# Kernel tuning notes

Measured on AMD Instinct MI355X. Metric: run time of the kernel, lower is better.

Reference implementation:

```python
import jax, jax.numpy as jnp
import numpy as np

N_NODES = 100000
IN_DIM = 128
N_HEADS = 4
D_HEAD = 32
N_EDGES = 800000
LN_EPS = 1e-5
NEG_SLOPE = 0.2


def setup_inputs() -> dict:
    key = jax.random.key(0)
    k = jax.random.split(key, 7)
    x = jax.random.normal(k[0], (N_NODES, IN_DIM), dtype=jnp.float32)
    edge_index = jax.random.randint(k[1], (2, N_EDGES), 0, N_NODES, dtype=jnp.int32)
    # W: Linear(in_dim, H*D, bias=False) -> store as [in_dim, H*D] for x @ W
    W = jax.random.normal(k[2], (IN_DIM, N_HEADS * D_HEAD), dtype=jnp.float32) * (1.0 / np.sqrt(IN_DIM))
    # attn_mlp: Linear(2*D, 1, bias=False), shared across heads; split into src/dst halves
    a_src = jax.random.normal(k[3], (D_HEAD,), dtype=jnp.float32) * 0.1
    a_dst = jax.random.normal(k[4], (D_HEAD,), dtype=jnp.float32) * 0.1
    ln_gamma = jnp.ones((N_HEADS * D_HEAD,), dtype=jnp.float32)
    ln_beta = jnp.zeros((N_HEADS * D_HEAD,), dtype=jnp.float32)
    return {"x": x, "edge_index": edge_index, "W": W, "a_src": a_src,
            "a_dst": a_dst, "ln_gamma": ln_gamma, "ln_beta": ln_beta}


def reference(x, edge_index, W, a_src, a_dst, ln_gamma, ln_beta):
    N = x.shape[0]
    # dense projection: [N, H*D] -> [N, H, D]
    h = (x @ W).reshape(N, N_HEADS, D_HEAD)
    src, dst = edge_index[0], edge_index[1]
    h_src = h[src]          # [E, H, D] gather
    h_dst = h[dst]          # [E, H, D] gather
    # attn_mlp(cat([h_src, h_dst])) == h_src @ a[:D] + h_dst @ a[D:]
    s = jnp.einsum('ehd,d->eh', h_src, a_src) + jnp.einsum('ehd,d->eh', h_dst, a_dst)
    s = jnp.where(s > 0, s, NEG_SLOPE * s)  # LeakyReLU(0.2)
    # segment softmax over destination node groups (per head)
    smax = jax.ops.segment_max(s, dst, num_segments=N)          # [N, H]
    e = jnp.exp(s - smax[dst])                                   # [E, H]
    denom = jax.ops.segment_sum(e, dst, num_segments=N)          # [N, H]
    alpha = e / denom[dst]                                       # [E, H]
    # weighted scatter-add aggregation
    msg = h_src * alpha[..., None]                               # [E, H, D]
    out = jax.ops.segment_sum(msg, dst, num_segments=N)          # [N, H, D]
    out = out.reshape(N, N_HEADS * D_HEAD)
    # residual: in_dim == H*D -> Identity
    out = out + x
    # LayerNorm
    mu = out.mean(-1, keepdims=True)
    var = ((out - mu) ** 2).mean(-1, keepdims=True)
    out = (out - mu) / jnp.sqrt(var + LN_EPS) * ln_gamma + ln_beta
    # ELU
    return jnp.where(out > 0, out, jnp.expm1(out))
```

## Files before the change

kernel.cpp:

```cpp
#include <hip/hip_runtime.h>
#include <math.h>

#define NEG_SLOPE 0.2f
#define LN_EPS 1e-5f

#define NB 196
#define EPB 2048

typedef __attribute__((ext_vector_type(8))) short bf16x8;
typedef __attribute__((ext_vector_type(4))) float f32x4;

static __device__ __forceinline__ unsigned short f2bf(float f) {
  unsigned u = __float_as_uint(f);
  u += 0x7fffu + ((u >> 16) & 1u);
  return (unsigned short)(u >> 16);
}
static __device__ __forceinline__ unsigned pack_bf16(float a, float b) {
  unsigned ua = __float_as_uint(a);
  unsigned ub = __float_as_uint(b);
  ua += 0x7fffu + ((ua >> 16) & 1u);
  ub += 0x7fffu + ((ub >> 16) & 1u);
  return (ua >> 16) | (ub & 0xffff0000u);
}
static __device__ __forceinline__ float bf_lo(unsigned u) { return __uint_as_float(u << 16); }
static __device__ __forceinline__ float bf_hi(unsigned u) { return __uint_as_float(u & 0xffff0000u); }

__global__ __launch_bounds__(256) void k_prep(
    const float* __restrict__ W, const float* __restrict__ a_src,
    const float* __restrict__ a_dst, short* __restrict__ wfrag,
    short* __restrict__ wafrag)
{
  const int t = threadIdx.x;
  if (blockIdx.x < 8) {
    const int idx  = blockIdx.x * 256 + t;
    const int tile = idx >> 6;
    const int l2   = idx & 63;
    const int c    = tile >> 2;
    const int kk   = tile & 3;
    const int q2   = l2 >> 4;
    const int i2   = l2 & 15;
    const float* wp = W + (size_t)(kk * 32 + q2 * 8) * 128 + c * 16 + i2;
    bf16x8 wv;
    #pragma unroll
    for (int j = 0; j < 8; ++j) wv[j] = (short)f2bf(wp[(size_t)j * 128]);
    *(bf16x8*)(wfrag + (size_t)idx * 8) = wv;
  } else {
    const int kk = t >> 6;
    const int l2 = t & 63;
    const int q2 = l2 >> 4;
    const int i2 = l2 & 15;
    bf16x8 wv = {0, 0, 0, 0, 0, 0, 0, 0};
    if (i2 < 8) {
      const int head = i2 >> 1;
      const float* ap = (i2 & 1) ? a_dst : a_src;
      #pragma unroll
      for (int j = 0; j < 8; ++j) {
        const int k = kk * 32 + q2 * 8 + j;
        const float* wr = W + (size_t)k * 128 + head * 32;
        float sum = 0.f;
        for (int d = 0; d < 32; d += 4) {
          const float4 wq = *(const float4*)(wr + d);
          const float4 aq = *(const float4*)(ap + d);
          sum += wq.x * aq.x + wq.y * aq.y + wq.z * aq.z + wq.w * aq.w;
        }
        wv[j] = (short)f2bf(sum);
      }
    }
    *(bf16x8*)(wafrag + (size_t)t * 8) = wv;
  }
}

__global__ __launch_bounds__(256) void k_bhist(
    const int* __restrict__ e_dst, int* __restrict__ H, int n_edges, int nblk)
{
  __shared__ int hist[NB];
  const int t = threadIdx.x;
  if (t < NB) hist[t] = 0;
  __syncthreads();
  int e = blockIdx.x * EPB + t * 8;
  if (e + 8 <= n_edges) {
    const int4 d0 = *(const int4*)(e_dst + e);
    const int4 d1 = *(const int4*)(e_dst + e + 4);
    atomicAdd(&hist[d0.x >> 9], 1); atomicAdd(&hist[d0.y >> 9], 1);
    atomicAdd(&hist[d0.z >> 9], 1); atomicAdd(&hist[d0.w >> 9], 1);
    atomicAdd(&hist[d1.x >> 9], 1); atomicAdd(&hist[d1.y >> 9], 1);
    atomicAdd(&hist[d1.z >> 9], 1); atomicAdd(&hist[d1.w >> 9], 1);
  } else {
    const int eend = (e + 8 < n_edges) ? (e + 8) : n_edges;
    for (; e < eend; ++e) atomicAdd(&hist[e_dst[e] >> 9], 1);
  }
  __syncthreads();
  if (t < NB) H[t * nblk + blockIdx.x] = hist[t];
}

__global__ __launch_bounds__(256) void k_cscan(
    int* __restrict__ H, int* __restrict__ totals, int nblk)
{
  __shared__ int sdata[256];
  const int b = blockIdx.x, t = threadIdx.x;
  int* col = H + (size_t)b * nblk;
  const int i0 = 2 * t, i1 = 2 * t + 1;
  const int v0 = (i0 < nblk) ? col[i0] : 0;
  const int v1 = (i1 < nblk) ? col[i1] : 0;
  const int tsum = v0 + v1;
  sdata[t] = tsum;
  __syncthreads();
  for (int off = 1; off < 256; off <<= 1) {
    const int addv = (t >= off) ? sdata[t - off] : 0;
    __syncthreads();
    sdata[t] += addv;
    __syncthreads();
  }
  const int excl = sdata[t] - tsum;
  if (i0 < nblk) col[i0] = excl;
  if (i1 < nblk) col[i1] = excl + v0;
  if (t == 255) totals[b] = sdata[255];
}

__global__ __launch_bounds__(256) void k_scatter(
    const int* __restrict__ e_src, const int* __restrict__ e_dst,
    const int* __restrict__ H, const int* __restrict__ totals,
    int2* __restrict__ ebuf, int n_edges, int nblk)
{
  __shared__ int sdata[256];
  __shared__ int cur[NB];
  const int t = threadIdx.x;
  const int tv = (t < NB) ? totals[t] : 0;
  sdata[t] = tv;
  __syncthreads();
  for (int off = 1; off < 256; off <<= 1) {
    const int addv = (t >= off) ? sdata[t - off] : 0;
    __syncthreads();
    sdata[t] += addv;
    __syncthreads();
  }
  if (t < NB) cur[t] = (sdata[t] - tv) + H[t * nblk + blockIdx.x];
  __syncthreads();
  int e = blockIdx.x * EPB + t * 8;
  if (e + 8 <= n_edges) {
    const int4 d0 = *(const int4*)(e_dst + e);
    const int4 d1 = *(const int4*)(e_dst + e + 4);
    const int4 s0 = *(const int4*)(e_src + e);
    const int4 s1 = *(const int4*)(e_src + e + 4);
    int p;
    p = atomicAdd(&cur[d0.x >> 9], 1); ebuf[p] = make_int2(d0.x, s0.x);
    p = atomicAdd(&cur[d0.y >> 9], 1); ebuf[p] = make_int2(d0.y, s0.y);
    p = atomicAdd(&cur[d0.z >> 9], 1); ebuf[p] = make_int2(d0.z, s0.z);
    p = atomicAdd(&cur[d0.w >> 9], 1); ebuf[p] = make_int2(d0.w, s0.w);
    p = atomicAdd(&cur[d1.x >> 9], 1); ebuf[p] = make_int2(d1.x, s1.x);
    p = atomicAdd(&cur[d1.y >> 9], 1); ebuf[p] = make_int2(d1.y, s1.y);
    p = atomicAdd(&cur[d1.z >> 9], 1); ebuf[p] = make_int2(d1.z, s1.z);
    p = atomicAdd(&cur[d1.w >> 9], 1); ebuf[p] = make_int2(d1.w, s1.w);
  } else {
    const int eend = (e + 8 < n_edges) ? (e + 8) : n_edges;
    for (; e < eend; ++e) {
      const int d = e_dst[e];
      const int p = atomicAdd(&cur[d >> 9], 1);
      ebuf[p] = make_int2(d, e_src[e]);
    }
  }
}

__global__ __launch_bounds__(256) void k_bcsr(
    const int2* __restrict__ ebuf, const int* __restrict__ totals,
    int* __restrict__ row_start, int* __restrict__ csr_src, int n_nodes)
{
  __shared__ int sdata[256];
  __shared__ int hist[512];
  __shared__ int cur[512];
  const int b = blockIdx.x, t = threadIdx.x;
  const int n0 = b << 9;

  const int tv = (t < NB) ? totals[t] : 0;
  sdata[t] = tv;
  __syncthreads();
  for (int off = 1; off < 256; off <<= 1) {
    const int addv = (t >= off) ? sdata[t - off] : 0;
    __syncthreads();
    sdata[t] += addv;
    __syncthreads();
  }
  const int base = (b == 0) ? 0 : sdata[b - 1];
  const int nE   = sdata[b] - base;

  hist[t] = 0; hist[t + 256] = 0;
  __syncthreads();
  for (int e = t; e < nE; e += 256)
    atomicAdd(&hist[ebuf[base + e].x - n0], 1);
  __syncthreads();

  const int h0 = hist[2 * t], h1 = hist[2 * t + 1];
  const int tsum = h0 + h1;
  sdata[t] = tsum;
  __syncthreads();
  for (int off = 1; off < 256; off <<= 1) {
    const int addv = (t >= off) ? sdata[t - off] : 0;
    __syncthreads();
    sdata[t] += addv;
    __syncthreads();
  }
  const int excl = sdata[t] - tsum;
  cur[2 * t]     = excl;
  cur[2 * t + 1] = excl + h0;
  if (n0 + 2 * t     <= n_nodes) row_start[n0 + 2 * t]     = base + excl;
  if (n0 + 2 * t + 1 <= n_nodes) row_start[n0 + 2 * t + 1] = base + excl + h0;
  __syncthreads();

  for (int e = t; e < nE; e += 256) {
    const int2 ds = ebuf[base + e];
    const int r = atomicAdd(&cur[ds.x - n0], 1);
    csr_src[base + r] = ds.y;
  }
}

__global__ __launch_bounds__(256, 4) void k_proj(
    const float* __restrict__ x, const short* __restrict__ wfrag,
    const short* __restrict__ wafrag,
    unsigned* __restrict__ h, float* __restrict__ sc, int n_nodes)
{
  __shared__ __align__(16) short wlds[32 * 64 * 8];
  __shared__ __align__(16) short walds[4 * 64 * 8];

  const int t    = threadIdx.x;
  const int l    = t & 63;
  const int il   = l & 15;
  const int quad = l >> 4;
  const int wbase = blockIdx.x * 128 + (t >> 6) * 32;

  {
    const uint4* wf4 = (const uint4*)wfrag;
    uint4* wl4 = (uint4*)wlds;
    #pragma unroll
    for (int i = 0; i < 8; ++i) wl4[t + i * 256] = wf4[t + i * 256];
    ((uint4*)walds)[t] = ((const uint4*)wafrag)[t];
  }
  __syncthreads();

  f32x4 acc[2][8] = {};
  f32x4 acc2[2] = {};
  #pragma unroll
  for (int kk = 0; kk < 4; ++kk) {
    bf16x8 ahi[2], alo[2];
    #pragma unroll
    for (int rt = 0; rt < 2; ++rt) {
      int row = wbase + rt * 16 + il;
      if (row > n_nodes - 1) row = n_nodes - 1;
      const float* p = x + (size_t)row * 128 + kk * 32 + quad * 8;
      const float4 u0 = *(const float4*)(p);
      const float4 u1 = *(const float4*)(p + 4);
      const float f[8] = {u0.x, u0.y, u0.z, u0.w, u1.x, u1.y, u1.z, u1.w};
      #pragma unroll
      for (int j = 0; j < 8; ++j) {
        const unsigned u = __float_as_uint(f[j]);
        ahi[rt][j] = (short)(u >> 16);
        const float lof = f[j] - __uint_as_float(u & 0xffff0000u);
        alo[rt][j] = (short)f2bf(lof);
      }
    }
    #pragma unroll
    for (int c = 0; c < 8; ++c) {
      const bf16x8 bv = *(const bf16x8*)(wlds + ((c * 4 + kk) * 64 + l) * 8);
      acc[0][c] = __builtin_amdgcn_mfma_f32_16x16x32_bf16(ahi[0], bv, acc[0][c], 0, 0, 0);
      acc[0][c] = __builtin_amdgcn_mfma_f32_16x16x32_bf16(alo[0], bv, acc[0][c], 0, 0, 0);
      acc[1][c] = __builtin_amdgcn_mfma_f32_16x16x32_bf16(ahi[1], bv, acc[1][c], 0, 0, 0);
      acc[1][c] = __builtin_amdgcn_mfma_f32_16x16x32_bf16(alo[1], bv, acc[1][c], 0, 0, 0);
    }
    const bf16x8 bv = *(const bf16x8*)(walds + (kk * 64 + l) * 8);
    acc2[0] = __builtin_amdgcn_mfma_f32_16x16x32_bf16(ahi[0], bv, acc2[0], 0, 0, 0);
    acc2[0] = __builtin_amdgcn_mfma_f32_16x16x32_bf16(alo[0], bv, acc2[0], 0, 0, 0);
    acc2[1] = __builtin_amdgcn_mfma_f32_16x16x32_bf16(ahi[1], bv, acc2[1], 0, 0, 0);
    acc2[1] = __builtin_amdgcn_mfma_f32_16x16x32_bf16(alo[1], bv, acc2[1], 0, 0, 0);
  }

  #pragma unroll
  for (int rt = 0; rt < 2; ++rt) {
    #pragma unroll
    for (int reg = 0; reg < 4; ++reg) {
      const int r = wbase + rt * 16 + quad * 4 + reg;
      const bool inb = (r < n_nodes);
      const bool wr = inb && ((il & 3) == 0);
      #pragma unroll
      for (int c = 0; c < 8; ++c) {
        const float v  = acc[rt][c][reg];
        const float vn = __shfl_xor(v, 1);
        const float plo = (il & 1) ? vn : v;
        const float phi = (il & 1) ? v : vn;
        const unsigned px = pack_bf16(plo, phi);
        const unsigned py = __shfl_xor(px, 2);
        if (wr) {
          uint2 u; u.x = px; u.y = py;
          *(uint2*)(h + (size_t)r * 64 + c * 8 + (il >> 1)) = u;
        }
      }
      if (inb && il < 8) sc[(size_t)r * 8 + il] = acc2[rt][reg];
    }
  }
}

#define ACC_EDGE(al, hv)                              \
  acc[0] = fmaf(al, bf_lo(hv.x), acc[0]);             \
  acc[1] = fmaf(al, bf_hi(hv.x), acc[1]);             \
  acc[2] = fmaf(al, bf_lo(hv.y), acc[2]);             \
  acc[3] = fmaf(al, bf_hi(hv.y), acc[3]);             \
  acc[4] = fmaf(al, bf_lo(hv.z), acc[4]);             \
  acc[5] = fmaf(al, bf_hi(hv.z), acc[5]);             \
  acc[6] = fmaf(al, bf_lo(hv.w), acc[6]);             \
  acc[7] = fmaf(al, bf_hi(hv.w), acc[7]);

__global__ __launch_bounds__(256) void k_agg(
    const unsigned* __restrict__ h, const float* __restrict__ sc,
    const int* __restrict__ row_start, const int* __restrict__ csr_src,
    const float* __restrict__ x, const float* __restrict__ gamma,
    const float* __restrict__ beta, float* __restrict__ out, int n_nodes)
{
  const int t    = threadIdx.x;
  const int lane = t & 63;
  const int g    = lane & 15;
  const int node = blockIdx.x * 16 + (t >> 6) * 4 + (lane >> 4);
  if (node >= n_nodes) return;
  const int head = g >> 2;
  const int sub  = g & 3;
  const int hh   = head * 2;
  const int beg  = row_start[node];
  const int deg  = row_start[node + 1] - beg;
  const float sdv = sc[node * 8 + hh + 1];

  float m = -INFINITY, l = 0.f;
  float t0 = 0.f, t1 = 0.f, t2 = 0.f, t3 = 0.f;
  int   c0 = 0,   c1 = 0,   c2 = 0,   c3 = 0;
  if (sub < deg) {
    c0 = csr_src[beg + sub];
    float s = sc[c0 * 8 + hh] + sdv;  s = s > 0.f ? s : NEG_SLOPE * s;
    t0 = s; m = s; l = 1.f;
  }
  if (sub + 4 < deg) {
    c1 = csr_src[beg + sub + 4];
    float s = sc[c1 * 8 + hh] + sdv;  s = s > 0.f ? s : NEG_SLOPE * s;
    t1 = s;
    const float mn = fmaxf(m, s);
    l = l * __expf(m - mn) + __expf(s - mn);  m = mn;
  }
  if (sub + 8 < deg) {
    c2 = csr_src[beg + sub + 8];
    float s = sc[c2 * 8 + hh] + sdv;  s = s > 0.f ? s : NEG_SLOPE * s;
    t2 = s;
    const float mn = fmaxf(m, s);
    l = l * __expf(m - mn) + __expf(s - mn);  m = mn;
  }
  if (sub + 12 < deg) {
    c3 = csr_src[beg + sub + 12];
    float s = sc[c3 * 8 + hh] + sdv;  s = s > 0.f ? s : NEG_SLOPE * s;
    t3 = s;
    const float mn = fmaxf(m, s);
    l = l * __expf(m - mn) + __expf(s - mn);  m = mn;
  }
  for (int i = sub + 16; i < deg; i += 4) {
    const int cs = csr_src[beg + i];
    float s = sc[cs * 8 + hh] + sdv;  s = s > 0.f ? s : NEG_SLOPE * s;
    const float mn = fmaxf(m, s);
    l = l * __expf(m - mn) + __expf(s - mn);  m = mn;
  }
  #pragma unroll
  for (int off = 1; off < 4; off <<= 1) {
    const float m2 = __shfl_xor(m, off);
    const float l2 = __shfl_xor(l, off);
    const float mn = fmaxf(m, m2);
    if (mn == -INFINITY) { m = -INFINITY; l = 0.f; }
    else {
      l = l * __expf(m - mn) + l2 * __expf(m2 - mn);
      m = mn;
    }
  }
  const float inv_l = (deg > 0) ? 1.f / l : 0.f;
  const float a0 = __expf(t0 - m) * inv_l;
  const float a1 = __expf(t1 - m) * inv_l;
  const float a2 = __expf(t2 - m) * inv_l;
  const float a3 = __expf(t3 - m) * inv_l;

  const int base3 = lane & 60;

  float acc[8] = {0.f, 0.f, 0.f, 0.f, 0.f, 0.f, 0.f, 0.f};
  const int deg16 = deg < 16 ? deg : 16;
  #pragma unroll
  for (int r = 0; r < 4; ++r) {
    const int i0 = r * 4;
    if (i0 >= deg16) break;
    const float ar = r == 0 ? a0 : r == 1 ? a1 : r == 2 ? a2 : a3;
    const int   cr = r == 0 ? c0 : r == 1 ? c1 : r == 2 ? c2 : c3;
    const int   n  = deg16 - i0;
    {
      const float al = __shfl(ar, base3 | 0);
      const int   sr = __shfl(cr, base3 | 0);
      const uint4 hv = *(const uint4*)(h + (size_t)sr * 64 + g * 4);
      ACC_EDGE(al, hv)
    }
    if (n > 1) {
      const float al = __shfl(ar, base3 | 1);
      const int   sr = __shfl(cr, base3 | 1);
      const uint4 hv = *(const uint4*)(h + (size_t)sr * 64 + g * 4);
      ACC_EDGE(al, hv)
    }
    if (n > 2) {
      const float al = __shfl(ar, base3 | 2);
      const int   sr = __shfl(cr, base3 | 2);
      const uint4 hv = *(const uint4*)(h + (size_t)sr * 64 + g * 4);
      ACC_EDGE(al, hv)
    }
    if (n > 3) {
      const float al = __shfl(ar, base3 | 3);
      const int   sr = __shfl(cr, base3 | 3);
      const uint4 hv = *(const uint4*)(h + (size_t)sr * 64 + g * 4);
      ACC_EDGE(al, hv)
    }
  }
  for (int i = 16; i < deg; ++i) {
    const int sr = csr_src[beg + i];
    float s = sc[sr * 8 + hh] + sdv;  s = s > 0.f ? s : NEG_SLOPE * s;
    const float al = __expf(s - m) * inv_l;
    const uint4 hv = *(const uint4*)(h + (size_t)sr * 64 + g * 4);
    ACC_EDGE(al, hv)
  }

  const float4 xa = *(const float4*)(x + (size_t)node * 128 + g * 8);
  const float4 xb = *(const float4*)(x + (size_t)node * 128 + g * 8 + 4);
  float rr[8];
  rr[0] = acc[0] + xa.x;  rr[1] = acc[1] + xa.y;
  rr[2] = acc[2] + xa.z;  rr[3] = acc[3] + xa.w;
  rr[4] = acc[4] + xb.x;  rr[5] = acc[5] + xb.y;
  rr[6] = acc[6] + xb.z;  rr[7] = acc[7] + xb.w;
  float s1 = 0.f, s2 = 0.f;
  #pragma unroll
  for (int j = 0; j < 8; ++j) { s1 += rr[j]; s2 += rr[j] * rr[j]; }
  #pragma unroll
  for (int off = 1; off < 16; off <<= 1) {
    s1 += __shfl_xor(s1, off);
    s2 += __shfl_xor(s2, off);
  }
  const float mu   = s1 * (1.f / 128.f);
  const float var  = s2 * (1.f / 128.f) - mu * mu;
  const float rstd = rsqrtf(var + LN_EPS);
  const float4 ga = *(const float4*)(gamma + g * 8);
  const float4 gb = *(const float4*)(gamma + g * 8 + 4);
  const float4 ba = *(const float4*)(beta  + g * 8);
  const float4 bb = *(const float4*)(beta  + g * 8 + 4);
  float4 o0, o1;
  o0.x = (rr[0] - mu) * rstd * ga.x + ba.x;
  o0.y = (rr[1] - mu) * rstd * ga.y + ba.y;
  o0.z = (rr[2] - mu) * rstd * ga.z + ba.z;
  o0.w = (rr[3] - mu) * rstd * ga.w + ba.w;
  o1.x = (rr[4] - mu) * rstd * gb.x + bb.x;
  o1.y = (rr[5] - mu) * rstd * gb.y + bb.y;
  o1.z = (rr[6] - mu) * rstd * gb.z + bb.z;
  o1.w = (rr[7] - mu) * rstd * gb.w + bb.w;
  o0.x = o0.x > 0.f ? o0.x : expm1f(o0.x);
  o0.y = o0.y > 0.f ? o0.y : expm1f(o0.y);
  o0.z = o0.z > 0.f ? o0.z : expm1f(o0.z);
  o0.w = o0.w > 0.f ? o0.w : expm1f(o0.w);
  o1.x = o1.x > 0.f ? o1.x : expm1f(o1.x);
  o1.y = o1.y > 0.f ? o1.y : expm1f(o1.y);
  o1.z = o1.z > 0.f ? o1.z : expm1f(o1.z);
  o1.w = o1.w > 0.f ? o1.w : expm1f(o1.w);
  *(float4*)(out + (size_t)node * 128 + g * 8)     = o0;
  *(float4*)(out + (size_t)node * 128 + g * 8 + 4) = o1;
}

extern "C" void kernel_launch(void* const* d_in, const int* in_sizes, int n_in,
                              void* d_out, int out_size, void* d_ws, size_t ws_size,
                              hipStream_t stream)
{
  const float* x    = (const float*)d_in[0];
  const int*   ei   = (const int*)d_in[1];
  const float* W    = (const float*)d_in[2];
  const float* a_s  = (const float*)d_in[3];
  const float* a_d  = (const float*)d_in[4];
  const float* gam  = (const float*)d_in[5];
  const float* bet  = (const float*)d_in[6];
  float* out = (float*)d_out;

  const int n_nodes = in_sizes[0] / 128;
  const int n_edges = in_sizes[1] / 2;
  const int* e_src = ei;
  const int* e_dst = ei + n_edges;

  const int nblkE = (n_edges + EPB - 1) / EPB;

  char* p = (char*)d_ws;
  unsigned* h = (unsigned*)p; p += (size_t)n_nodes * 64 * sizeof(unsigned);
  float* sc   = (float*)p;  p += (size_t)n_nodes * 8 * sizeof(float);
  int* row_start = (int*)p; p += (size_t)(n_nodes + 4) * sizeof(int);
  int* csr_src   = (int*)p; p += (size_t)n_edges * sizeof(int);
  short* wfrag   = (short*)p; p += (size_t)2048 * 8 * sizeof(short);
  short* wafrag  = (short*)p; p += (size_t)256 * 8 * sizeof(short);
  int* H      = (int*)p; p += (size_t)NB * nblkE * sizeof(int);
  int* totals = (int*)p; p += (size_t)NB * sizeof(int);
  int2* ebuf  = (int2*)h;

  k_prep<<<9, 256, 0, stream>>>(W, a_s, a_d, wfrag, wafrag);
  k_bhist<<<nblkE, 256, 0, stream>>>(e_dst, H, n_edges, nblkE);
  k_cscan<<<NB, 256, 0, stream>>>(H, totals, nblkE);
  k_scatter<<<nblkE, 256, 0, stream>>>(e_src, e_dst, H, totals, ebuf, n_edges, nblkE);
  k_bcsr<<<NB, 256, 0, stream>>>(ebuf, totals, row_start, csr_src, n_nodes);
  const int nproj = (n_nodes + 127) / 128;
  k_proj<<<nproj, 256, 0, stream>>>(x, wfrag, wafrag, h, sc, n_nodes);
  k_agg<<<(n_nodes + 15) / 16, 256, 0, stream>>>(h, sc, row_start, csr_src, x, gam, bet, out, n_nodes);
}
```

Baseline: 207.5 us.

## Fuse CSR build and projection into one cooperative kernel; two-pass softmax

Merges the prep, histogram, scan, scatter, per-bucket CSR and projection kernels into a single cooperative persistent kernel that separates phases with grid-wide syncs and reuses one shared-memory buffer. The aim is to remove several kernel launch gaps and tail effects. The projection tiles now run in a grid-stride loop over a fixed grid, which may cause load imbalance. The aggregation kernel swaps its online softmax for a max pass then a sum pass, which trades the rescaling exps for a second gather of neighbour scores. It also uses nontemporal loads for x and nontemporal stores for the output.

Measured after the change: 476.3 us. +129.5%, slower.

```diff
diff --git a/kernel.cpp b/kernel.cpp
--- a/kernel.cpp
+++ b/kernel.cpp
@@ -1,4 +1,5 @@
 #include <hip/hip_runtime.h>
+#include <hip/hip_cooperative_groups.h>
 #include <math.h>
 
 #define NEG_SLOPE 0.2f
@@ -6,6 +7,9 @@
 
 #define NB 196
 #define EPB 2048
+#define SMEM_BYTES (36 * 1024)
+
+namespace cg = cooperative_groups;
 
 typedef __attribute__((ext_vector_type(8))) short bf16x8;
 typedef __attribute__((ext_vector_type(4))) float f32x4;
@@ -25,14 +29,15 @@
 static __device__ __forceinline__ float bf_lo(unsigned u) { return __uint_as_float(u << 16); }
 static __device__ __forceinline__ float bf_hi(unsigned u) { return __uint_as_float(u & 0xffff0000u); }
 
-__global__ __launch_bounds__(256) void k_prep(
+
+static __device__ __forceinline__ void prep_body(
     const float* __restrict__ W, const float* __restrict__ a_src,
     const float* __restrict__ a_dst, short* __restrict__ wfrag,
-    short* __restrict__ wafrag)
+    short* __restrict__ wafrag, int bid)
 {
   const int t = threadIdx.x;
-  if (blockIdx.x < 8) {
-    const int idx  = blockIdx.x * 256 + t;
+  if (bid < 8) {
+    const int idx  = bid * 256 + t;
     const int tile = idx >> 6;
     const int l2   = idx & 63;
     const int c    = tile >> 2;
@@ -70,14 +75,15 @@
   }
 }
 
-__global__ __launch_bounds__(256) void k_bhist(
-    const int* __restrict__ e_dst, int* __restrict__ H, int n_edges, int nblk)
-{
-  __shared__ int hist[NB];
+static __device__ __forceinline__ void bhist_body(
+    const int* __restrict__ e_dst, int* __restrict__ H, int n_edges, int nblk,
+    int b, char* smem)
+{
+  int* hist = (int*)smem;
   const int t = threadIdx.x;
   if (t < NB) hist[t] = 0;
   __syncthreads();
-  int e = blockIdx.x * EPB + t * 8;
+  int e = b * EPB + t * 8;
   if (e + 8 <= n_edges) {
     const int4 d0 = *(const int4*)(e_dst + e);
     const int4 d1 = *(const int4*)(e_dst + e + 4);
@@ -90,14 +96,14 @@
     for (; e < eend; ++e) atomicAdd(&hist[e_dst[e] >> 9], 1);
   }
   __syncthreads();
-  if (t < NB) H[t * nblk + blockIdx.x] = hist[t];
-}
-
-__global__ __launch_bounds__(256) void k_cscan(
-    int* __restrict__ H, int* __restrict__ totals, int nblk)
-{
-  __shared__ int sdata[256];
-  const int b = blockIdx.x, t = threadIdx.x;
+  if (t < NB) H[t * nblk + b] = hist[t];
+}
+
+static __device__ __forceinline__ void cscan_body(
+    int* __restrict__ H, int* __restrict__ totals, int nblk, int b, char* smem)
+{
+  int* sdata = (int*)smem;
+  const int t = threadIdx.x;
   int* col = H + (size_t)b * nblk;
   const int i0 = 2 * t, i1 = 2 * t + 1;
   const int v0 = (i0 < nblk) ? col[i0] : 0;
@@ -117,13 +123,13 @@
   if (t == 255) totals[b] = sdata[255];
 }
 
-__global__ __launch_bounds__(256) void k_scatter(
+static __device__ __forceinline__ void scatter_body(
     const int* __restrict__ e_src, const int* __restrict__ e_dst,
     const int* __restrict__ H, const int* __restrict__ totals,
-    int2* __restrict__ ebuf, int n_edges, int nblk)
-{
-  __shared__ int sdata[256];
-  __shared__ int cur[NB];
+    int2* __restrict__ ebuf, int n_edges, int nblk, int b, char* smem)
+{
+  int* sdata = (int*)smem;
+  int* cur   = (int*)(smem + 1024);
   const int t = threadIdx.x;
   const int tv = (t < NB) ? totals[t] : 0;
   sdata[t] = tv;
@@ -134,9 +140,9 @@
     sdata[t] += addv;
     __syncthreads();
   }
-  if (t < NB) cur[t] = (sdata[t] - tv) + H[t * nblk + blockIdx.x];
-  __syncthreads();
-  int e = blockIdx.x * EPB + t * 8;
+  if (t < NB) cur[t] = (sdata[t] - tv) + H[t * nblk + b];
+  __syncthreads();
+  int e = b * EPB + t * 8;
   if (e + 8 <= n_edges) {
     const int4 d0 = *(const int4*)(e_dst + e);
     const int4 d1 = *(const int4*)(e_dst + e + 4);
@@ -161,14 +167,15 @@
   }
 }
 
-__global__ __launch_bounds__(256) void k_bcsr(
+static __device__ __forceinline__ void bcsr_body(
     const int2* __restrict__ ebuf, const int* __restrict__ totals,
-    int* __restrict__ row_start, int* __restrict__ csr_src, int n_nodes)
-{
-  __shared__ int sdata[256];
-  __shared__ int hist[512];
-  __shared__ int cur[512];
-  const int b = blockIdx.x, t = threadIdx.x;
+    int* __restrict__ row_start, int* __restrict__ csr_src, int n_nodes,
+    int b, char* smem)
+{
+  int* sdata = (int*)smem;
+  int* hist  = (int*)(smem + 1024);
+  int* cur   = (int*)(smem + 1024 + 2048);
+  const int t = threadIdx.x;
   const int n0 = b << 9;
 
   const int tv = (t < NB) ? totals[t] : 0;
@@ -213,28 +220,32 @@
   }
 }
 
-__global__ __launch_bounds__(256, 4) void k_proj(
-    const float* __restrict__ x, const short* __restrict__ wfrag,
-    const short* __restrict__ wafrag,
-    unsigned* __restrict__ h, float* __restrict__ sc, int n_nodes)
-{
-  __shared__ __align__(16) short wlds[32 * 64 * 8];
-  __shared__ __align__(16) short walds[4 * 64 * 8];
+static __device__ __forceinline__ void proj_stage(
+    const short* __restrict__ wfrag, const short* __restrict__ wafrag,
+    char* smem)
+{
+  short* wlds  = (short*)smem;
+  short* walds = (short*)(smem + 32 * 1024);
+  const int t = threadIdx.x;
+  const uint4* wf4 = (const uint4*)wfrag;
+  uint4* wl4 = (uint4*)wlds;
+  #pragma unroll
+  for (int i = 0; i < 8; ++i) wl4[t + i * 256] = wf4[t + i * 256];
+  ((uint4*)walds)[t] = ((const uint4*)wafrag)[t];
+}
+
+static __device__ __forceinline__ void proj_compute(
+    const float* __restrict__ x, unsigned* __restrict__ h,
+    float* __restrict__ sc, int n_nodes, int pb, char* smem)
+{
+  short* wlds  = (short*)smem;
+  short* walds = (short*)(smem + 32 * 1024);
 
   const int t    = threadIdx.x;
   const int l    = t & 63;
   const int il   = l & 15;
   const int quad = l >> 4;
-  const int wbase = blockIdx.x * 128 + (t >> 6) * 32;
-
-  {
-    const uint4* wf4 = (const uint4*)wfrag;
-    uint4* wl4 = (uint4*)wlds;
-    #pragma unroll
-    for (int i = 0; i < 8; ++i) wl4[t + i * 256] = wf4[t + i * 256];
-    ((uint4*)walds)[t] = ((const uint4*)wafrag)[t];
-  }
-  __syncthreads();
+  const int wbase = pb * 128 + (t >> 6) * 32;
 
   f32x4 acc[2][8] = {};
   f32x4 acc2[2] = {};
@@ -297,6 +308,41 @@
   }
 }
 
+__global__ __launch_bounds__(256, 4) void k_csrproj(
+    const float* __restrict__ W, const float* __restrict__ a_src,
+    const float* __restrict__ a_dst, short* __restrict__ wfrag,
+    short* __restrict__ wafrag,
+    const int* __restrict__ e_src, const int* __restrict__ e_dst,
+    int* __restrict__ H, int* __restrict__ totals, int2* __restrict__ ebuf,
+    int* __restrict__ row_start, int* __restrict__ csr_src,
+    const float* __restrict__ x, unsigned* __restrict__ h,
+    float* __restrict__ sc, int n_nodes, int n_edges, int nblk, int nproj)
+{
+  __shared__ __align__(16) char smem[SMEM_BYTES];
+  cg::grid_group grid = cg::this_grid();
+
+  if ((int)blockIdx.x < 9) prep_body(W, a_src, a_dst, wfrag, wafrag, blockIdx.x);
+  else if ((int)blockIdx.x < 9 + nblk)
+    bhist_body(e_dst, H, n_edges, nblk, blockIdx.x - 9, smem);
+  grid.sync();
+
+  if ((int)blockIdx.x < NB) cscan_body(H, totals, nblk, blockIdx.x, smem);
+  grid.sync();
+
+  if ((int)blockIdx.x < nblk)
+    scatter_body(e_src, e_dst, H, totals, ebuf, n_edges, nblk, blockIdx.x, smem);
+  grid.sync();
+
+  if ((int)blockIdx.x < NB)
+    bcsr_body(ebuf, totals, row_start, csr_src, n_nodes, blockIdx.x, smem);
+  grid.sync();
+
+  proj_stage(wfrag, wafrag, smem);
+  __syncthreads();
+  for (int u = blockIdx.x; u < nproj; u += gridDim.x)
+    proj_compute(x, h, sc, n_nodes, u, smem);
+}
+
 #define ACC_EDGE(al, hv)                              \
   acc[0] = fmaf(al, bf_lo(hv.x), acc[0]);             \
   acc[1] = fmaf(al, bf_hi(hv.x), acc[1]);             \
@@ -325,57 +371,48 @@
   const int deg  = row_start[node + 1] - beg;
   const float sdv = sc[node * 8 + hh + 1];
 
-  float m = -INFINITY, l = 0.f;
-  float t0 = 0.f, t1 = 0.f, t2 = 0.f, t3 = 0.f;
-  int   c0 = 0,   c1 = 0,   c2 = 0,   c3 = 0;
+  float t0 = -INFINITY, t1 = -INFINITY, t2 = -INFINITY, t3 = -INFINITY;
+  int   c0 = 0,          c1 = 0,          c2 = 0,          c3 = 0;
   if (sub < deg) {
     c0 = csr_src[beg + sub];
-    float s = sc[c0 * 8 + hh] + sdv;  s = s > 0.f ? s : NEG_SLOPE * s;
-    t0 = s; m = s; l = 1.f;
+    float s = sc[c0 * 8 + hh] + sdv;  t0 = s > 0.f ? s : NEG_SLOPE * s;
   }
   if (sub + 4 < deg) {
     c1 = csr_src[beg + sub + 4];
-    float s = sc[c1 * 8 + hh] + sdv;  s = s > 0.f ? s : NEG_SLOPE * s;
-    t1 = s;
-    const float mn = fmaxf(m, s);
-    l = l * __expf(m - mn) + __expf(s - mn);  m = mn;
+    float s = sc[c1 * 8 + hh] + sdv;  t1 = s > 0.f ? s : NEG_SLOPE * s;
   }
   if (sub + 8 < deg) {
     c2 = csr_src[beg + sub + 8];
-    float s = sc[c2 * 8 + hh] + sdv;  s = s > 0.f ? s : NEG_SLOPE * s;
-    t2 = s;
-    const float mn = fmaxf(m, s);
-    l = l * __expf(m - mn) + __expf(s - mn);  m = mn;
+    float s = sc[c2 * 8 + hh] + sdv;  t2 = s > 0.f ? s : NEG_SLOPE * s;
   }
   if (sub + 12 < deg) {
     c3 = csr_src[beg + sub + 12];
-    float s = sc[c3 * 8 + hh] + sdv;  s = s > 0.f ? s : NEG_SLOPE * s;
-    t3 = s;
-    const float mn = fmaxf(m, s);
-    l = l * __expf(m - mn) + __expf(s - mn);  m = mn;
-  }
+    float s = sc[c3 * 8 + hh] + sdv;  t3 = s > 0.f ? s : NEG_SLOPE * s;
+  }
+  float m = fmaxf(fmaxf(t0, t1), fmaxf(t2, t3));
   for (int i = sub + 16; i < deg; i += 4) {
     const int cs = csr_src[beg + i];
     float s = sc[cs * 8 + hh] + sdv;  s = s > 0.f ? s : NEG_SLOPE * s;
-    const float mn = fmaxf(m, s);
-    l = l * __expf(m - mn) + __expf(s - mn);  m = mn;
-  }
-  #pragma unroll
-  for (int off = 1; off < 4; off <<= 1) {
-    const float m2 = __shfl_xor(m, off);
-    const float l2 = __shfl_xor(l, off);
-    const float mn = fmaxf(m, m2);
-    if (mn == -INFINITY) { m = -INFINITY; l = 0.f; }
-    else {
-      l = l * __expf(m - mn) + l2 * __expf(m2 - mn);
-      m = mn;
-    }
-  }
+    m = fmaxf(m, s);
+  }
+  m = fmaxf(m, __shfl_xor(m, 1));
+  m = fmaxf(m, __shfl_xor(m, 2));
+
+  const float e0 = __expf(t0 - m), e1 = __expf(t1 - m);
+  const float e2 = __expf(t2 - m), e3 = __expf(t3 - m);
+  float l = e0 + e1 + e2 + e3;
+  for (int i = sub + 16; i < deg; i += 4) {
+    const int cs = csr_src[beg + i];
+    float s = sc[cs * 8 + hh] + sdv;  s = s > 0.f ? s : NEG_SLOPE * s;
+    l += __expf(s - m);
+  }
+  l += __shfl_xor(l, 1);
+  l += __shfl_xor(l, 2);
   const float inv_l = (deg > 0) ? 1.f / l : 0.f;
-  const float a0 = __expf(t0 - m) * inv_l;
-  const float a1 = __expf(t1 - m) * inv_l;
-  const float a2 = __expf(t2 - m) * inv_l;
-  const float a3 = __expf(t3 - m) * inv_l;
+  const float a0 = e0 * inv_l;
+  const float a1 = e1 * inv_l;
+  const float a2 = e2 * inv_l;
+  const float a3 = e3 * inv_l;
 
   const int base3 = lane & 60;
 
@@ -421,13 +458,13 @@
     ACC_EDGE(al, hv)
   }
 
-  const float4 xa = *(const float4*)(x + (size_t)node * 128 + g * 8);
-  const float4 xb = *(const float4*)(x + (size_t)node * 128 + g * 8 + 4);
+  const f32x4 xa = __builtin_nontemporal_load((const f32x4*)(x + (size_t)node * 128 + g * 8));
+  const f32x4 xb = __builtin_nontemporal_load((const f32x4*)(x + (size_t)node * 128 + g * 8 + 4));
   float rr[8];
-  rr[0] = acc[0] + xa.x;  rr[1] = acc[1] + xa.y;
-  rr[2] = acc[2] + xa.z;  rr[3] = acc[3] + xa.w;
-  rr[4] = acc[4] + xb.x;  rr[5] = acc[5] + xb.y;
-  rr[6] = acc[6] + xb.z;  rr[7] = acc[7] + xb.w;
+  rr[0] = acc[0] + xa[0];  rr[1] = acc[1] + xa[1];
+  rr[2] = acc[2] + xa[2];  rr[3] = acc[3] + xa[3];
+  rr[4] = acc[4] + xb[0];  rr[5] = acc[5] + xb[1];
+  rr[6] = acc[6] + xb[2];  rr[7] = acc[7] + xb[3];
   float s1 = 0.f, s2 = 0.f;
   #pragma unroll
   for (int j = 0; j < 8; ++j) { s1 += rr[j]; s2 += rr[j] * rr[j]; }
@@ -443,25 +480,25 @@
   const float4 gb = *(const float4*)(gamma + g * 8 + 4);
   const float4 ba = *(const float4*)(beta  + g * 8);
   const float4 bb = *(const float4*)(beta  + g * 8 + 4);
-  float4 o0, o1;
-  o0.x = (rr[0] - mu) * rstd * ga.x + ba.x;
-  o0.y = (rr[1] - mu) * rstd * ga.y + ba.y;
-  o0.z = (rr[2] - mu) * rstd * ga.z + ba.z;
-  o0.w = (rr[3] - mu) * rstd * ga.w + ba.w;
-  o1.x = (rr[4] - mu) * rstd * gb.x + bb.x;
-  o1.y = (rr[5] - mu) * rstd * gb.y + bb.y;
-  o1.z = (rr[6] - mu) * rstd * gb.z + bb.z;
-  o1.w = (rr[7] - mu) * rstd * gb.w + bb.w;
-  o0.x = o0.x > 0.f ? o0.x : expm1f(o0.x);
-  o0.y = o0.y > 0.f ? o0.y : expm1f(o0.y);
-  o0.z = o0.z > 0.f ? o0.z : expm1f(o0.z);
-  o0.w = o0.w > 0.f ? o0.w : expm1f(o0.w);
-  o1.x = o1.x > 0.f ? o1.x : expm1f(o1.x);
-  o1.y = o1.y > 0.f ? o1.y : expm1f(o1.y);
-  o1.z = o1.z > 0.f ? o1.z : expm1f(o1.z);
-  o1.w = o1.w > 0.f ? o1.w : expm1f(o1.w);
-  *(float4*)(out + (size_t)node * 128 + g * 8)     = o0;
-  *(float4*)(out + (size_t)node * 128 + g * 8 + 4) = o1;
+  f32x4 o0, o1;
+  o0[0] = (rr[0] - mu) * rstd * ga.x + ba.x;
+  o0[1] = (rr[1] - mu) * rstd * ga.y + ba.y;
+  o0[2] = (rr[2] - mu) * rstd * ga.z + ba.z;
+  o0[3] = (rr[3] - mu) * rstd * ga.w + ba.w;
+  o1[0] = (rr[4] - mu) * rstd * gb.x + bb.x;
+  o1[1] = (rr[5] - mu) * rstd * gb.y + bb.y;
+  o1[2] = (rr[6] - mu) * rstd * gb.z + bb.z;
+  o1[3] = (rr[7] - mu) * rstd * gb.w + bb.w;
+  o0[0] = o0[0] > 0.f ? o0[0] : expm1f(o0[0]);
+  o0[1] = o0[1] > 0.f ? o0[1] : expm1f(o0[1]);
+  o0[2] = o0[2] > 0.f ? o0[2] : expm1f(o0[2]);
+  o0[3] = o0[3] > 0.f ? o0[3] : expm1f(o0[3]);
+  o1[0] = o1[0] > 0.f ? o1[0] : expm1f(o1[0]);
+  o1[1] = o1[1] > 0.f ? o1[1] : expm1f(o1[1]);
+  o1[2] = o1[2] > 0.f ? o1[2] : expm1f(o1[2]);
+  o1[3] = o1[3] > 0.f ? o1[3] : expm1f(o1[3]);
+  __builtin_nontemporal_store(o0, (f32x4*)(out + (size_t)node * 128 + g * 8));
+  __builtin_nontemporal_store(o1, (f32x4*)(out + (size_t)node * 128 + g * 8 + 4));
 }
 
 extern "C" void kernel_launch(void* const* d_in, const int* in_sizes, int n_in,
@@ -483,6 +520,7 @@
   const int* e_dst = ei + n_edges;
 
   const int nblkE = (n_edges + EPB - 1) / EPB;
+  const int nproj = (n_nodes + 127) / 128;
 
   char* p = (char*)d_ws;
   unsigned* h = (unsigned*)p; p += (size_t)n_nodes * 64 * sizeof(unsigned);
@@ -492,15 +530,22 @@
   short* wfrag   = (short*)p; p += (size_t)2048 * 8 * sizeof(short);
   short* wafrag  = (short*)p; p += (size_t)256 * 8 * sizeof(short);
   int* H      = (int*)p; p += (size_t)NB * nblkE * sizeof(int);
-  int* totals = (int*)p; p += (size_t)NB * sizeof(int);
+  int* totals = (int*)p; p += (size_t)((NB + 3) & ~3) * sizeof(int);
   int2* ebuf  = (int2*)h;
 
-  k_prep<<<9, 256, 0, stream>>>(W, a_s, a_d, wfrag, wafrag);
-  k_bhist<<<nblkE, 256, 0, stream>>>(e_dst, H, n_edges, nblkE);
-  k_cscan<<<NB, 256, 0, stream>>>(H, totals, nblkE);
-  k_scatter<<<nblkE, 256, 0, stream>>>(e_src, e_dst, H, totals, ebuf, n_edges, nblkE);
-  k_bcsr<<<NB, 256, 0, stream>>>(ebuf, totals, row_start, csr_src, n_nodes);
-  const int nproj = (n_nodes + 127) / 128;
-  k_proj<<<nproj, 256, 0, stream>>>(x, wfrag, wafrag, h, sc, n_nodes);
-  k_agg<<<(n_nodes + 15) / 16, 256, 0, stream>>>(h, sc, row_start, csr_src, x, gam, bet, out, n_nodes);
-}
+  int ngrid = 9 + nblkE;
+  if (ngrid < 512) ngrid = 512;
+
+  int n_nodes_v = n_nodes, n_edges_v = n_edges, nblk_v = nblkE, nproj_v = nproj;
+  void* args[] = {
+    (void*)&W, (void*)&a_s, (void*)&a_d, (void*)&wfrag, (void*)&wafrag,
+    (void*)&e_src, (void*)&e_dst, (void*)&H, (void*)&totals, (void*)&ebuf,
+    (void*)&row_start, (void*)&csr_src, (void*)&x, (void*)&h, (void*)&sc,
+    (void*)&n_nodes_v, (void*)&n_edges_v, (void*)&nblk_v, (void*)&nproj_v
+  };
+  hipLaunchCooperativeKernel((const void*)k_csrproj, dim3(ngrid), dim3(256),
+                             args, 0, stream);
+
+  k_agg<<<(n_nodes + 15) / 16, 256, 0, stream>>>(h, sc, row_start, csr_src,
+                                                 x, gam, bet, out, n_nodes);
+}
```
